# Performance work log

Hardware: AMD Instinct MI355X
Metric: run time of the kernel (lower is better)

## Reference

```python
import jax, jax.numpy as jnp
import numpy as np
from jax import lax

N, D, BATCH = 8192, 256, 64


def setup_inputs() -> dict:
    key = jax.random.key(0)
    V = jax.random.normal(key, (N, D), dtype=jnp.float32)
    V = V / jnp.linalg.norm(V, axis=1, keepdims=True)  # cosine = raw dot product
    return {
        "V": V,
        "cos_threshold": jnp.array([0.25], dtype=jnp.float32),
        "batch_size": BATCH,
    }


def reference(V, cos_threshold, batch_size):
    """Faithful port of Embeddings._fast_predict: batched cosine-sim thresholding
    followed by a sequential transitive merge of group ids.

    Returns group_ids [N] int32 (the clustering result; the torch code wraps this
    into a Matcher object, which is pure python bookkeeping).
    """
    n, d = V.shape
    B = int(batch_size)
    n_batches = n // B
    thr = cos_threshold[0]
    j_idx = jnp.arange(n, dtype=jnp.int32)
    group_init = jnp.arange(n, dtype=jnp.int32)

    def outer(gids, batch_start):
        # group ids as of the start of this batch (torch computes batch_matched
        # with these, but reads live group_ids inside the row loop via views)
        g0 = gids
        Vb = lax.dynamic_slice(V, (batch_start, 0), (B, d))        # [B, D]
        sims = Vb @ V.T                                            # [B, N]
        g0_i = lax.dynamic_slice(g0, (batch_start,), (B,))         # [B]
        jmask = j_idx > batch_start                                # j_slice = batch_start+1 .. N
        mask = (sims >= thr) & jmask[None, :] & (g0_i[:, None] != g0[None, :])  # [B, N]

        def inner(g, inp):
            k, row = inp
            gi = g[batch_start + k]  # live group id of row i (torch g_i is a view)
            # isin(group_ids, matched_groups): flag[label]=1 if any matched j has
            # current group label == label, then gather back through g
            flag = jnp.zeros(n, jnp.int32).at[g].max(row.astype(jnp.int32))
            g = jnp.where(flag[g] > 0, gi, g)
            return g, None

        gids, _ = lax.scan(inner, gids, (jnp.arange(B, dtype=jnp.int32), mask))
        return gids, None

    starts = jnp.arange(n_batches, dtype=jnp.int32) * B
    gids, _ = lax.scan(outer, group_init, starts)
    return gids
```

## Files before the change

### kernel.cpp

```cpp
#include <hip/hip_runtime.h>
#include <stdint.h>

#define NPTS 8192
#define DIM  256
#define CAP  32768
#define LDSE 8192
#define IBCAP 256
#define BAND 2.0e-3f

typedef _Float16 f16x8  __attribute__((ext_vector_type(8)));
typedef float    f32x16 __attribute__((ext_vector_type(16)));


__global__ __launch_bounds__(256) void convert_kernel(
        const float* __restrict__ V, _Float16* __restrict__ Vh,
        unsigned* __restrict__ ctr) {
    if (blockIdx.x == 0 && threadIdx.x == 0) { ctr[0] = 0u; ctr[1] = 0u; }
    size_t t = (size_t)blockIdx.x * 256 + threadIdx.x;
    const float4* src = reinterpret_cast<const float4*>(V) + t * 2;
    float4 v0 = src[0], v1 = src[1];
    f16x8 h;
    h[0] = (_Float16)v0.x; h[1] = (_Float16)v0.y;
    h[2] = (_Float16)v0.z; h[3] = (_Float16)v0.w;
    h[4] = (_Float16)v1.x; h[5] = (_Float16)v1.y;
    h[6] = (_Float16)v1.z; h[7] = (_Float16)v1.w;
    *reinterpret_cast<f16x8*>(Vh + t * 8) = h;
}

__global__ void init_count(unsigned* ctr) {
    if (threadIdx.x == 0) { ctr[0] = 0u; ctr[1] = 0u; }
}

__device__ __forceinline__ void gload_lds16(const void* g, void* l) {
    __builtin_amdgcn_global_load_lds(
        (const __attribute__((address_space(1))) void*)g,
        (__attribute__((address_space(3))) void*)l, 16, 0, 0);
}

__global__ __launch_bounds__(512, 2) void edge_mfma(
        const _Float16* __restrict__ Vh,
        const float* __restrict__ V,
        const float* __restrict__ thr_p,
        unsigned* __restrict__ ctr,
        unsigned* __restrict__ edges) {
    int t = blockIdx.x;
    int bi = (int)(32.5f - sqrtf(32.5f * 32.5f - 2.0f * (float)t));
    while (bi * 32 - (bi * (bi - 1)) / 2 > t) --bi;
    while ((bi + 1) * 32 - ((bi + 1) * bi) / 2 <= t) ++bi;
    int bj = bi + (t - (bi * 32 - (bi * (bi - 1)) / 2));

    __shared__ _Float16 L[2][32768];
    __shared__ unsigned ibl[IBCAP];
    __shared__ unsigned ibn;

    const float thr = thr_p[0];
    const float hi = thr + BAND, lo = thr - BAND;
    const int tid  = threadIdx.x;
    const int lane = tid & 63;
    const int wid  = tid >> 6;
    const int wr = wid >> 2, wc = wid & 3;
    const int i0 = bi * 256, j0 = bj * 256;

    if (tid == 0) ibn = 0u;

    f32x16 acc[4][2];
#pragma unroll
    for (int a = 0; a < 4; ++a)
#pragma unroll
        for (int b = 0; b < 2; ++b) acc[a][b] = 0.0f;

    const int row_l = lane >> 3;
    const int bphys = lane & 7;
    const int l31 = lane & 31, g = lane >> 5, l7 = lane & 7;
    const int cblk = bphys ^ row_l;

    auto STAGE = [&](int buf, int kc) {
#pragma unroll
        for (int q = 0; q < 8; ++q) {
            const int qq  = wid * 8 + q;
            const int arr = qq >> 5;
            const int ins = qq & 31;
            const int grow = (arr ? j0 : i0) + ins * 8 + row_l;
            gload_lds16(Vh + ((size_t)grow * DIM + kc + cblk * 8),
                        &L[buf][arr * 16384 + ins * 512]);
        }
    };

    auto COMPUTE = [&](int buf) {
#pragma unroll
        for (int s = 0; s < 4; ++s) {
            const int xa = (((s * 2 + g) ^ l7) << 3);
            f16x8 af[4], bf[2];
#pragma unroll
            for (int a = 0; a < 4; ++a)
                af[a] = *(const f16x8*)&L[buf][(wr * 128 + a * 32 + l31) * 64 + xa];
#pragma unroll
            for (int b = 0; b < 2; ++b)
                bf[b] = *(const f16x8*)&L[buf][16384 + (wc * 64 + b * 32 + l31) * 64 + xa];
#pragma unroll
            for (int a = 0; a < 4; ++a)
#pragma unroll
                for (int b = 0; b < 2; ++b)
                    acc[a][b] = __builtin_amdgcn_mfma_f32_32x32x16_f16(
                        af[a], bf[b], acc[a][b], 0, 0, 0);
        }
    };

    STAGE(0, 0);
    __syncthreads();
    STAGE(1, 64);  COMPUTE(0); __syncthreads();
    STAGE(0, 128); COMPUTE(1); __syncthreads();
    STAGE(1, 192); COMPUTE(0); __syncthreads();
    COMPUTE(1);
    __syncthreads();

#pragma unroll
    for (int a = 0; a < 4; ++a)
#pragma unroll
        for (int b = 0; b < 2; ++b)
#pragma unroll
            for (int reg = 0; reg < 16; ++reg) {
                float sim = acc[a][b][reg];
                int rr = (reg & 3) + 8 * (reg >> 2) + 4 * g;
                int i = i0 + wr * 128 + a * 32 + rr;
                int j = j0 + wc * 64 + b * 32 + l31;
                if (j > i && sim >= lo) {
                    unsigned key = ((unsigned)i << 13) | (unsigned)j;
                    if (sim >= hi) {
                        unsigned p = atomicAdd(&ctr[0], 1u);
                        if (p < CAP) edges[p] = key;
                    } else {
                        unsigned p = atomicAdd(&ibn, 1u);
                        if (p < IBCAP) ibl[p] = key;
                    }
                }
            }
    __syncthreads();

    unsigned nib = ibn; if (nib > IBCAP) nib = IBCAP;
    const double thrd = (double)thr;
    for (unsigned q = tid; q < nib; q += 512) {
        unsigned key = ibl[q];
        int i = (int)(key >> 13), j = (int)(key & 8191u);
        const float4* a4 = reinterpret_cast<const float4*>(V + (size_t)i * DIM);
        const float4* b4 = reinterpret_cast<const float4*>(V + (size_t)j * DIM);
        double s = 0.0;
#pragma unroll 4
        for (int k = 0; k < DIM / 4; ++k) {
            float4 x = a4[k], y = b4[k];
            s += (double)x.x * y.x + (double)x.y * y.y
               + (double)x.z * y.z + (double)x.w * y.w;
        }
        if (s >= thrd) {
            unsigned p = atomicAdd(&ctr[0], 1u);
            if (p < CAP) edges[p] = key;
        }
    }
}

__global__ __launch_bounds__(256) void edge_kernel(
        const float* __restrict__ V,
        const float* __restrict__ thr_p,
        unsigned*    __restrict__ ctr,
        unsigned*    __restrict__ edges) {
    const int bi = blockIdx.y, bj = blockIdx.x;
    if (bj < bi) return;

    __shared__ float As[128 * 32];
    __shared__ float Bs[128 * 32];

    const float thr = thr_p[0];
    const int tid = threadIdx.x;
    const int tx = tid & 15, ty = tid >> 4;
    const int i0 = bi * 128, j0 = bj * 128;

    float acc[8][8];
#pragma unroll
    for (int r = 0; r < 8; ++r)
#pragma unroll
        for (int c = 0; c < 8; ++c) acc[r][c] = 0.f;

    const int srow = tid >> 3, sq = tid & 7;

    for (int kc = 0; kc < DIM; kc += 32) {
#pragma unroll
        for (int p = 0; p < 4; ++p) {
            int row = srow + 32 * p;
            float4 va = *reinterpret_cast<const float4*>(
                &V[(size_t)(i0 + row) * DIM + kc + sq * 4]);
            float4 vb = *reinterpret_cast<const float4*>(
                &V[(size_t)(j0 + row) * DIM + kc + sq * 4]);
            int w = row * 32 + ((sq ^ ((row >> 3) & 7)) << 2);
            *reinterpret_cast<float4*>(&As[w]) = va;
            *reinterpret_cast<float4*>(&Bs[w]) = vb;
        }
        __syncthreads();
#pragma unroll
        for (int k4 = 0; k4 < 8; ++k4) {
            const float* pA = &As[(ty * 8) * 32 + ((k4 ^ (ty & 7)) << 2)];
            const float* pB = &Bs[(tx * 8) * 32 + ((k4 ^ (tx & 7)) << 2)];
            float4 a[8], b[8];
#pragma unroll
            for (int r = 0; r < 8; ++r)
                a[r] = *reinterpret_cast<const float4*>(&pA[r * 32]);
#pragma unroll
            for (int c = 0; c < 8; ++c)
                b[c] = *reinterpret_cast<const float4*>(&pB[c * 32]);
#pragma unroll
            for (int r = 0; r < 8; ++r)
#pragma unroll
                for (int c = 0; c < 8; ++c) {
                    acc[r][c] = fmaf(a[r].x, b[c].x, acc[r][c]);
                    acc[r][c] = fmaf(a[r].y, b[c].y, acc[r][c]);
                    acc[r][c] = fmaf(a[r].z, b[c].z, acc[r][c]);
                    acc[r][c] = fmaf(a[r].w, b[c].w, acc[r][c]);
                }
        }
        __syncthreads();
    }
#pragma unroll
    for (int r = 0; r < 8; ++r)
#pragma unroll
        for (int c = 0; c < 8; ++c) {
            int i = i0 + ty * 8 + r;
            int j = j0 + tx * 8 + c;
            if (j > i && acc[r][c] >= thr) {
                unsigned p = atomicAdd(&ctr[0], 1u);
                if (p < CAP) edges[p] = ((unsigned)i << 13) | (unsigned)j;
            }
        }
}

__global__ __launch_bounds__(1024) void uf_kernel(
        const unsigned* __restrict__ ctr,
        const unsigned* __restrict__ edges,
        int* __restrict__ out) {
    __shared__ int      par[NPTS];
    __shared__ unsigned slotA[NPTS];
    __shared__ unsigned slotB[NPTS];
    __shared__ unsigned sedge[LDSE];

    const int tid = threadIdx.x;

    unsigned EC = ctr[0]; if (EC > LDSE) EC = LDSE;

    for (int t = tid; t < NPTS; t += 1024) {
        par[t] = t; slotA[t] = 0xFFFFFFFFu; slotB[t] = 0xFFFFFFFFu;
    }
    for (unsigned e = tid; e < EC; e += 1024) sedge[e] = edges[e];
    __syncthreads();

    volatile int* vpar = par;

    for (int round = 0;; ++round) {
        unsigned* S = (round & 1) ? slotB : slotA;
        unsigned* T = (round & 1) ? slotA : slotB;

        for (unsigned e = tid; e < EC; e += 1024) {
            unsigned key = sedge[e];
            if (key & 0x80000000u) continue;
            int ri = (int)(key >> 13), rj = (int)(key & 8191u);
            int p;
            while ((p = vpar[ri]) != ri) ri = p;
            while ((p = vpar[rj]) != rj) rj = p;
            atomicMin(&S[ri], key);
            atomicMin(&S[rj], key);
        }
        __syncthreads();

        int mylive = 0;
        for (unsigned e = tid; e < EC; e += 1024) {
            unsigned key = sedge[e];
            if (key & 0x80000000u) continue;
            int i = (int)(key >> 13), j = (int)(key & 8191u);
            int ri = i, rj = j, p;
            while ((p = vpar[ri]) != ri) ri = p;
            while ((p = vpar[rj]) != rj) rj = p;
            if (S[ri] == key && S[rj] == key) {
                if (ri != rj) { par[rj] = ri; par[i] = ri; par[j] = ri; }
                sedge[e] = key | 0x80000000u;
            } else {
                mylive = 1;
            }
        }
        for (int t = tid; t < NPTS; t += 1024) T[t] = 0xFFFFFFFFu;
        if (__syncthreads_count(mylive) == 0) break;
    }

    for (int t = tid; t < NPTS; t += 1024) {
        int r = t, p;
        while ((p = par[r]) != r) r = p;
        out[t] = r;
    }
}

extern "C" void kernel_launch(void* const* d_in, const int* in_sizes, int n_in,
                              void* d_out, int out_size, void* d_ws, size_t ws_size,
                              hipStream_t stream) {
    const float* V     = (const float*)d_in[0];
    const float* thr_p = (const float*)d_in[1];

    unsigned* ctr   = (unsigned*)d_ws;
    unsigned* edges = (unsigned*)((char*)d_ws + 64);
    int*      out   = (int*)d_out;

    const size_t vhOff = 1u << 20;
    const size_t vN    = (size_t)NPTS * DIM;
    const size_t need  = vhOff + vN * sizeof(_Float16) + 65536;

    if (ws_size >= need) {
        _Float16* Vh = (_Float16*)((char*)d_ws + vhOff);
        hipLaunchKernelGGL(convert_kernel, dim3(1024), dim3(256), 0, stream,
                           V, Vh, ctr);
        hipLaunchKernelGGL(edge_mfma, dim3(528), dim3(512), 0, stream,
                           Vh, V, thr_p, ctr, edges);
    } else {
        hipLaunchKernelGGL(init_count, dim3(1), dim3(64), 0, stream, ctr);
        hipLaunchKernelGGL(edge_kernel, dim3(64, 64), dim3(256), 0, stream,
                           V, thr_p, ctr, edges);
    }
    hipLaunchKernelGGL(uf_kernel, dim3(1), dim3(1024), 0, stream,
                       ctr, edges, out);
}
```

Measured before the change: 108.7 us.

## Shrink edge GEMM tiles to 256x128 with 256 threads and 32-wide K chunks

The similarity kernel now uses 256x128 output tiles computed by 4 waves instead of 256x256 tiles on 8 waves. The grid grows to 1056 blocks, with a matching triangular block-index mapping. K is staged in 32-wide chunks over an 8-step double-buffered loop, which cuts LDS per block from about 128KB to 48KB so more blocks can be resident per CU and the work spreads more evenly. The cost is that the XOR swizzle on the LDS layout is gone, so fragment reads may hit bank conflicts, and each loaded tile is reused less.

```diff
diff --git a/kernel.cpp b/kernel.cpp
--- a/kernel.cpp
+++ b/kernel.cpp
@@ -37,19 +37,21 @@
         (__attribute__((address_space(3))) void*)l, 16, 0, 0);
 }
 
-__global__ __launch_bounds__(512, 2) void edge_mfma(
+__global__ __launch_bounds__(256, 2) void edge_mfma(
         const _Float16* __restrict__ Vh,
         const float* __restrict__ V,
         const float* __restrict__ thr_p,
         unsigned* __restrict__ ctr,
         unsigned* __restrict__ edges) {
     int t = blockIdx.x;
-    int bi = (int)(32.5f - sqrtf(32.5f * 32.5f - 2.0f * (float)t));
-    while (bi * 32 - (bi * (bi - 1)) / 2 > t) --bi;
-    while ((bi + 1) * 32 - ((bi + 1) * bi) / 2 <= t) ++bi;
-    int bj = bi + (t - (bi * 32 - (bi * (bi - 1)) / 2));
-
-    __shared__ _Float16 L[2][32768];
+    int bi = (int)((65.0f - sqrtf(4225.0f - 4.0f * (float)t)) * 0.5f);
+    if (bi > 31) bi = 31;
+    while (bi > 0 && bi * (65 - bi) > t) --bi;
+    while ((bi + 1) * (64 - bi) <= t) ++bi;
+    int bj = 2 * bi + (t - bi * (65 - bi));
+
+    __shared__ _Float16 LA[2][256 * 32];
+    __shared__ _Float16 LB[2][128 * 32];
     __shared__ unsigned ibl[IBCAP];
     __shared__ unsigned ibn;
 
@@ -58,8 +60,8 @@
     const int tid  = threadIdx.x;
     const int lane = tid & 63;
     const int wid  = tid >> 6;
-    const int wr = wid >> 2, wc = wid & 3;
-    const int i0 = bi * 256, j0 = bj * 256;
+    const int wr = wid >> 1, wc = wid & 1;
+    const int i0 = bi * 256, j0 = bj * 128;
 
     if (tid == 0) ibn = 0u;
 
@@ -69,34 +71,38 @@
 #pragma unroll
         for (int b = 0; b < 2; ++b) acc[a][b] = 0.0f;
 
-    const int row_l = lane >> 3;
-    const int bphys = lane & 7;
-    const int l31 = lane & 31, g = lane >> 5, l7 = lane & 7;
-    const int cblk = bphys ^ row_l;
+    const int l31 = lane & 31, g = lane >> 5;
+    const int srow = lane >> 2;
+    const int sblk = lane & 3;
 
     auto STAGE = [&](int buf, int kc) {
 #pragma unroll
-        for (int q = 0; q < 8; ++q) {
-            const int qq  = wid * 8 + q;
-            const int arr = qq >> 5;
-            const int ins = qq & 31;
-            const int grow = (arr ? j0 : i0) + ins * 8 + row_l;
-            gload_lds16(Vh + ((size_t)grow * DIM + kc + cblk * 8),
-                        &L[buf][arr * 16384 + ins * 512]);
+        for (int q = 0; q < 6; ++q) {
+            const int qq = wid * 6 + q;
+            if (qq < 16) {
+                const int grow = i0 + qq * 16 + srow;
+                gload_lds16(Vh + ((size_t)grow * DIM + kc + sblk * 8),
+                            &LA[buf][qq * 512]);
+            } else {
+                const int ins = qq - 16;
+                const int grow = j0 + ins * 16 + srow;
+                gload_lds16(Vh + ((size_t)grow * DIM + kc + sblk * 8),
+                            &LB[buf][ins * 512]);
+            }
         }
     };
 
     auto COMPUTE = [&](int buf) {
 #pragma unroll
-        for (int s = 0; s < 4; ++s) {
-            const int xa = (((s * 2 + g) ^ l7) << 3);
+        for (int s = 0; s < 2; ++s) {
+            const int xo = s * 16 + g * 8;
             f16x8 af[4], bf[2];
 #pragma unroll
             for (int a = 0; a < 4; ++a)
-                af[a] = *(const f16x8*)&L[buf][(wr * 128 + a * 32 + l31) * 64 + xa];
+                af[a] = *(const f16x8*)&LA[buf][(wr * 128 + a * 32 + l31) * 32 + xo];
 #pragma unroll
             for (int b = 0; b < 2; ++b)
-                bf[b] = *(const f16x8*)&L[buf][16384 + (wc * 64 + b * 32 + l31) * 64 + xa];
+                bf[b] = *(const f16x8*)&LB[buf][(wc * 64 + b * 32 + l31) * 32 + xo];
 #pragma unroll
             for (int a = 0; a < 4; ++a)
 #pragma unroll
@@ -108,11 +114,12 @@
 
     STAGE(0, 0);
     __syncthreads();
-    STAGE(1, 64);  COMPUTE(0); __syncthreads();
-    STAGE(0, 128); COMPUTE(1); __syncthreads();
-    STAGE(1, 192); COMPUTE(0); __syncthreads();
-    COMPUTE(1);
-    __syncthreads();
+#pragma unroll
+    for (int it = 0; it < 8; ++it) {
+        if (it < 7) STAGE((it + 1) & 1, (it + 1) * 32);
+        COMPUTE(it & 1);
+        __syncthreads();
+    }
 
 #pragma unroll
     for (int a = 0; a < 4; ++a)
@@ -139,7 +146,7 @@
 
     unsigned nib = ibn; if (nib > IBCAP) nib = IBCAP;
     const double thrd = (double)thr;
-    for (unsigned q = tid; q < nib; q += 512) {
+    for (unsigned q = tid; q < nib; q += 256) {
         unsigned key = ibl[q];
         int i = (int)(key >> 13), j = (int)(key & 8191u);
         const float4* a4 = reinterpret_cast<const float4*>(V + (size_t)i * DIM);
@@ -312,7 +319,7 @@
         _Float16* Vh = (_Float16*)((char*)d_ws + vhOff);
         hipLaunchKernelGGL(convert_kernel, dim3(1024), dim3(256), 0, stream,
                            V, Vh, ctr);
-        hipLaunchKernelGGL(edge_mfma, dim3(528), dim3(512), 0, stream,
+        hipLaunchKernelGGL(edge_mfma, dim3(1056), dim3(256), 0, stream,
                            Vh, V, thr_p, ctr, edges);
     } else {
         hipLaunchKernelGGL(init_count, dim3(1), dim3(64), 0, stream, ctr);
```

Result: faster. 103.7 us (-4.7%).
